# Optimization experiments

Measured on AMD Instinct MI355X. Metric: run time of the kernel, lower is better.

## Reference

```python
import jax, jax.numpy as jnp
import numpy as np

IN_SIZE = 128
OUT_SIZE = 128
NEG_SLOPE = 0.01  # flax.nnx.leaky_relu default


def setup_inputs() -> dict:
    key = jax.random.key(0)
    x = jax.random.normal(key, (8, IN_SIZE, IN_SIZE, 128), dtype=jnp.float32)
    return {"x": x}


def reference(x) -> jnp.ndarray:
    b, _, _, c = x.shape
    x = jax.image.resize(x, (b, 2 * IN_SIZE, 2 * IN_SIZE, c), method='bicubic', antialias=True)
    # filtered nonlinearity
    x = jax.nn.leaky_relu(x, negative_slope=NEG_SLOPE)
    # bicubic antialiased downsample back to out_size
    x = jax.image.resize(x, (b, OUT_SIZE, OUT_SIZE, c), method='bicubic', antialias=True)
    return x
```

## Files before the change

kernel.cpp:

```cpp
#include <hip/hip_runtime.h>

typedef float f2 __attribute__((ext_vector_type(2)));
typedef float f4 __attribute__((ext_vector_type(4)));

#define IN_H 128
#define IN_W 128
#define NCH  128
#define UPN  256

constexpr int SEG  = 8;
constexpr int COLS = 32;
constexpr int CH   = 32;
constexpr int IRW  = 14;
constexpr int ICW  = 38;
constexpr int NT4  = IRW * ICW * CH / 4;

__device__ __forceinline__ float cubic_k(float x) {
  float r = 0.f;
  if (x < 1.f)      r = (1.5f * x - 2.5f) * x * x + 1.f;
  else if (x < 2.f) r = ((-0.5f * x + 2.5f) * x - 4.f) * x + 2.f;
  return r;
}

#define GLDS(g, l)                                                         \
  __builtin_amdgcn_global_load_lds(                                        \
      (const __attribute__((address_space(1))) void*)(g),                  \
      (__attribute__((address_space(3))) void*)(l), 16, 0, 0)

__global__ __launch_bounds__(256, 2)
void actfilter_kernel(const float* __restrict__ x, float* __restrict__ out) {
  __shared__ __align__(16) float xin[IRW][ICW][CH];
  __shared__ __align__(16) float upw[UPN][4];
  __shared__ __align__(16) float dww[IN_H][8];

  const int tid = threadIdx.x;

  int bid  = blockIdx.x;
  int work = ((bid & 7) << 8) | (bid >> 3);
  const int b   = work >> 8;
  const int rs  = (work >> 4) & 15;
  const int cs  = (work >> 2) & 3;
  const int chs = work & 3;
  const int i0  = rs * SEG;
  const int jc0 = cs * COLS;
  const int c0  = chs * CH;
  const int mlo = i0 - 3;
  const int mhi = i0 + 10;

  const float* xbase = x   + (size_t)b * IN_H * IN_W * NCH;
  float*       obase = out + (size_t)b * IN_H * IN_W * NCH;

  {
    char* lbase = (char*)&xin[0][0][0] + ((tid >> 6) << 10);
#pragma unroll
    for (int pass = 0; pass < 17; ++pass) {
      int t = tid + pass * 256;
      if (t < NT4) {
        int row   = t / 304;
        int rem   = t - row * 304;
        int col   = rem >> 3;
        int piece = rem & 7;
        int gr = min(max(mlo + row, 0), IN_H - 1);
        int gc = min(max(jc0 - 3 + col, 0), IN_W - 1);
        const float* gp = xbase + ((size_t)gr * IN_W + gc) * NCH + c0 + piece * 4;
        GLDS(gp, lbase + pass * 4096);
      }
    }
  }

  {
    int o = tid;
    int k = o >> 1;
    int base = (o & 1) ? (k - 1) : (k - 2);
    float s = 0.5f * o - 0.25f;
    float w[4]; float sum = 0.f;
#pragma unroll
    for (int t = 0; t < 4; ++t) {
      int tap = base + t;
      float wt = (tap >= 0 && tap < IN_H) ? cubic_k(fabsf(s - (float)tap)) : 0.f;
      w[t] = wt; sum += wt;
    }
    float inv = 1.f / sum;
#pragma unroll
    for (int t = 0; t < 4; ++t) upw[o][t] = w[t] * inv;
  }
  if (tid < IN_H) {
    int j = tid;
    float s = 2.f * j + 0.5f;
    float w[8]; float sum = 0.f;
#pragma unroll
    for (int t = 0; t < 8; ++t) {
      int tap = 2 * j - 3 + t;
      float wt = (tap >= 0 && tap < UPN) ? cubic_k(0.5f * fabsf(s - (float)tap)) : 0.f;
      w[t] = wt; sum += wt;
    }
    float inv = 1.f / sum;
#pragma unroll
    for (int t = 0; t < 8; ++t) dww[j][t] = w[t] * inv;
  }

  __syncthreads();

  const int cp = tid >> 4;
  const int e  = tid & 15;
  const int j0 = jc0 + 2 * cp;

  f4 wvv[10];
#pragma unroll
  for (int c = 0; c < 10; ++c) {
    int cu = min(max(2 * j0 - 3 + c, 0), UPN - 1);
    wvv[c] = *(const f4*)&upw[cu][0];
  }
  float dw0[8], dw1[8];
  {
    f4 a = *(const f4*)&dww[j0][0],     bq = *(const f4*)&dww[j0][4];
    f4 c2 = *(const f4*)&dww[j0 + 1][0], d = *(const f4*)&dww[j0 + 1][4];
#pragma unroll
    for (int t = 0; t < 4; ++t) {
      dw0[t] = a[t]; dw0[t + 4] = bq[t];
      dw1[t] = c2[t]; dw1[t + 4] = d[t];
    }
  }

  const int r_lo = max(2 * i0 - 3, 0);
  const int r_hi = min(2 * i0 + 2 * SEG + 2, UPN - 1);

  const f4 whE = {-0.0234375f, 0.2265625f, 0.8671875f, -0.0703125f};
  const f4 whO = {-0.0703125f, 0.8671875f, 0.2265625f, -0.0234375f};

  f2 tw[4][10];
  f2 accA[4], accB[4];
#pragma unroll
  for (int s2 = 0; s2 < 4; ++s2) {
    accA[s2] = (f2){0.f, 0.f};
    accB[s2] = (f2){0.f, 0.f};
  }

#define DO_R(RV, WHC, S0, S1, S2, S3)                                        \
  do {                                                                       \
    int r = (RV);                                                            \
    if (r >= r_lo && r <= r_hi) {                                            \
      f4 wh = (WHC);                                                         \
      if (r < 3 || r > 252) wh = *(const f4*)&upw[r][0];                     \
      f2 z0 = (f2){0.f, 0.f}, z1 = (f2){0.f, 0.f};                           \
      _Pragma("unroll")                                                      \
      for (int c = 0; c < 10; ++c) {                                         \
        f2 hu = wh.x * tw[S0][c] + wh.y * tw[S1][c]                          \
              + wh.z * tw[S2][c] + wh.w * tw[S3][c];                         \
        f2 lv;                                                               \
        lv.x = fmaxf(hu.x, 0.01f * hu.x);                                    \
        lv.y = fmaxf(hu.y, 0.01f * hu.y);                                    \
        if (c < 8)  z0 += dw0[c] * lv;                                       \
        if (c >= 2) z1 += dw1[c - 2] * lv;                                   \
      }                                                                      \
      int ilo = max(i0, (r - 3) >> 1);                                       \
      int ihi = min(i0 + SEG - 1, (r + 3) >> 1);                             \
      _Pragma("unroll")                                                      \
      for (int s = 0; s < 4; ++s) {                                          \
        int i = ilo + ((s - ilo) & 3);                                       \
        if (i <= ihi) {                                                      \
          float w = dww[i][r - 2 * i + 3];                                   \
          accA[s] += w * z0;                                                 \
          accB[s] += w * z1;                                                 \
          bool done = (r == 2 * i + 4) ||                                    \
                      (r == UPN - 1 && 2 * i + 4 > UPN - 1);                 \
          if (done) {                                                        \
            float* dst = obase + ((size_t)i * IN_W + j0) * NCH + c0 + 2 * e; \
            *(f2*)dst         = accA[s];                                     \
            *(f2*)(dst + NCH) = accB[s];                                     \
            accA[s] = (f2){0.f, 0.f};                                        \
            accB[s] = (f2){0.f, 0.f};                                        \
          }                                                                  \
        }                                                                    \
      }                                                                      \
    }                                                                        \
  } while (0)

#define STEP(PH)                                                             \
  do {                                                                       \
    int m = mlo + mb + (PH);                                                 \
    if (m <= mhi) {                                                          \
      int ml = m - mlo;                                                      \
      f2 raw[8];                                                             \
      _Pragma("unroll")                                                      \
      for (int k = 0; k < 8; ++k)                                            \
        raw[k] = *(const f2*)&xin[ml][2 * cp + k][2 * e];                    \
      _Pragma("unroll")                                                      \
      for (int c = 0; c < 10; ++c) {                                         \
        tw[(PH) & 3][c] = wvv[c].x * raw[(c >> 1) + 0]                       \
                        + wvv[c].y * raw[(c >> 1) + 1]                       \
                        + wvv[c].z * raw[(c >> 1) + 2]                       \
                        + wvv[c].w * raw[(c >> 1) + 3];                      \
      }                                                                      \
      DO_R(2 * m - 3, whO, ((PH) + 1) & 3, ((PH) + 2) & 3, ((PH) + 3) & 3, (PH) & 3); \
      DO_R(2 * m - 2, whE, ((PH) + 1) & 3, ((PH) + 2) & 3, ((PH) + 3) & 3, (PH) & 3); \
    }                                                                        \
  } while (0)

  for (int mb = 0; mb < 16; mb += 4) {
    STEP(0);
    STEP(1);
    STEP(2);
    STEP(3);
  }

#undef STEP
#undef DO_R
}

extern "C" void kernel_launch(void* const* d_in, const int* in_sizes, int n_in,
                              void* d_out, int out_size, void* d_ws, size_t ws_size,
                              hipStream_t stream) {
  const float* x = (const float*)d_in[0];
  float* out = (float*)d_out;
  actfilter_kernel<<<dim3(2048), dim3(256), 0, stream>>>(x, out);
}
```

Before: 76.34 us.

## Stage input tile in LDS as fp16 via register loads with padded rows

Replaces the direct global-to-LDS async loads with register loads that convert the input to packed fp16 (round-toward-zero) before storing to a padded LDS tile. The loads are staged in batches interleaved with the weight-table setup to overlap latency. The intent is to halve LDS footprint and read bandwidth, possibly improving occupancy and reducing bank conflicts. It adds conversion instructions and register pressure, and loses precision by converting inputs to fp16, which may violate accuracy tolerance.

```diff
diff --git a/kernel.cpp b/kernel.cpp
--- a/kernel.cpp
+++ b/kernel.cpp
@@ -2,6 +2,7 @@
 
 typedef float f2 __attribute__((ext_vector_type(2)));
 typedef float f4 __attribute__((ext_vector_type(4)));
+typedef _Float16 h2 __attribute__((ext_vector_type(2)));
 
 #define IN_H 128
 #define IN_W 128
@@ -11,9 +12,11 @@
 constexpr int SEG  = 8;
 constexpr int COLS = 32;
 constexpr int CH   = 32;
+constexpr int CHP  = 38;
 constexpr int IRW  = 14;
 constexpr int ICW  = 38;
 constexpr int NT4  = IRW * ICW * CH / 4;
+constexpr int TPR  = ICW * CH / 4;
 
 __device__ __forceinline__ float cubic_k(float x) {
   float r = 0.f;
@@ -22,14 +25,14 @@
   return r;
 }
 
-#define GLDS(g, l)                                                         \
-  __builtin_amdgcn_global_load_lds(                                        \
-      (const __attribute__((address_space(1))) void*)(g),                  \
-      (__attribute__((address_space(3))) void*)(l), 16, 0, 0)
+__device__ __forceinline__ h2 pkrtz(float a, float b) {
+  auto t = __builtin_amdgcn_cvt_pkrtz(a, b);
+  return __builtin_bit_cast(h2, t);
+}
 
 __global__ __launch_bounds__(256, 2)
 void actfilter_kernel(const float* __restrict__ x, float* __restrict__ out) {
-  __shared__ __align__(16) float xin[IRW][ICW][CH];
+  __shared__ __align__(16) _Float16 xin[IRW][ICW][CHP];
   __shared__ __align__(16) float upw[UPN][4];
   __shared__ __align__(16) float dww[IN_H][8];
 
@@ -50,23 +53,44 @@
   const float* xbase = x   + (size_t)b * IN_H * IN_W * NCH;
   float*       obase = out + (size_t)b * IN_H * IN_W * NCH;
 
-  {
-    char* lbase = (char*)&xin[0][0][0] + ((tid >> 6) << 10);
-#pragma unroll
-    for (int pass = 0; pass < 17; ++pass) {
-      int t = tid + pass * 256;
-      if (t < NT4) {
-        int row   = t / 304;
-        int rem   = t - row * 304;
-        int col   = rem >> 3;
-        int piece = rem & 7;
-        int gr = min(max(mlo + row, 0), IN_H - 1);
-        int gc = min(max(jc0 - 3 + col, 0), IN_W - 1);
-        const float* gp = xbase + ((size_t)gr * IN_W + gc) * NCH + c0 + piece * 4;
-        GLDS(gp, lbase + pass * 4096);
+  auto ldb = [&](int base, int cnt, f4* v) {
+#pragma unroll
+    for (int k = 0; k < 6; ++k) {
+      if (k < cnt) {
+        int t = tid + (base + k) * 256;
+        if (t < NT4) {
+          int row   = t / TPR;
+          int rem   = t - row * TPR;
+          int col   = rem >> 3;
+          int piece = rem & 7;
+          int gr = min(max(mlo + row, 0), IN_H - 1);
+          int gc = min(max(jc0 - 3 + col, 0), IN_W - 1);
+          v[k] = *(const f4*)(xbase + ((size_t)gr * IN_W + gc) * NCH
+                              + c0 + piece * 4);
+        }
       }
     }
-  }
+  };
+  auto stb = [&](int base, int cnt, const f4* v) {
+#pragma unroll
+    for (int k = 0; k < 6; ++k) {
+      if (k < cnt) {
+        int t = tid + (base + k) * 256;
+        if (t < NT4) {
+          int row   = t / TPR;
+          int rem   = t - row * TPR;
+          int col   = rem >> 3;
+          int piece = rem & 7;
+          _Float16* lp = &xin[row][col][piece * 4];
+          *(h2*)lp       = pkrtz(v[k].x, v[k].y);
+          *(h2*)(lp + 2) = pkrtz(v[k].z, v[k].w);
+        }
+      }
+    }
+  };
+
+  f4 sA[6], sB[6];
+  ldb(0, 6, sA);
 
   {
     int o = tid;
@@ -84,6 +108,10 @@
 #pragma unroll
     for (int t = 0; t < 4; ++t) upw[o][t] = w[t] * inv;
   }
+
+  ldb(6, 6, sB);
+  stb(0, 6, sA);
+
   if (tid < IN_H) {
     int j = tid;
     float s = 2.f * j + 0.5f;
@@ -98,6 +126,10 @@
 #pragma unroll
     for (int t = 0; t < 8; ++t) dww[j][t] = w[t] * inv;
   }
+
+  ldb(12, 5, sA);
+  stb(6, 6, sB);
+  stb(12, 5, sA);
 
   __syncthreads();
 
@@ -183,8 +215,11 @@
       int ml = m - mlo;                                                      \
       f2 raw[8];                                                             \
       _Pragma("unroll")                                                      \
-      for (int k = 0; k < 8; ++k)                                            \
-        raw[k] = *(const f2*)&xin[ml][2 * cp + k][2 * e];                    \
+      for (int k = 0; k < 8; ++k) {                                          \
+        h2 rv = *(const h2*)&xin[ml][2 * cp + k][2 * e];                     \
+        raw[k].x = (float)rv.x;                                              \
+        raw[k].y = (float)rv.y;                                              \
+      }                                                                      \
       _Pragma("unroll")                                                      \
       for (int c = 0; c < 10; ++c) {                                         \
         tw[(PH) & 3][c] = wvv[c].x * raw[(c >> 1) + 0]                       \
```

Result: slower. 80.26 us (+5.1%).

## Remap threads to one channel by four output columns for wider horizontal reuse

Applied to the files above, without the earlier changes.

Each thread now handles one channel and four consecutive output columns instead of two channels by two columns. The horizontal upsample row of 14 taps is shared across four downsample outputs, so less of it is recomputed between neighbouring columns (10 taps per 2 columns before, 14 per 4 now). The cost is more registers per thread (tw grows to 4x14 and the accumulators to 4x4), which may lower occupancy. Loads and stores also become scalar and strided across columns instead of float2.

```diff
diff --git a/kernel.cpp b/kernel.cpp
--- a/kernel.cpp
+++ b/kernel.cpp
@@ -1,6 +1,5 @@
 #include <hip/hip_runtime.h>
 
-typedef float f2 __attribute__((ext_vector_type(2)));
 typedef float f4 __attribute__((ext_vector_type(4)));
 
 #define IN_H 128
@@ -101,25 +100,23 @@
 
   __syncthreads();
 
-  const int cp = tid >> 4;
-  const int e  = tid & 15;
-  const int j0 = jc0 + 2 * cp;
-
-  f4 wvv[10];
-#pragma unroll
-  for (int c = 0; c < 10; ++c) {
+  const int cp = tid >> 5;
+  const int e  = tid & 31;
+  const int j0 = jc0 + 4 * cp;
+
+  f4 wvv[14];
+#pragma unroll
+  for (int c = 0; c < 14; ++c) {
     int cu = min(max(2 * j0 - 3 + c, 0), UPN - 1);
     wvv[c] = *(const f4*)&upw[cu][0];
   }
-  float dw0[8], dw1[8];
-  {
-    f4 a = *(const f4*)&dww[j0][0],     bq = *(const f4*)&dww[j0][4];
-    f4 c2 = *(const f4*)&dww[j0 + 1][0], d = *(const f4*)&dww[j0 + 1][4];
-#pragma unroll
-    for (int t = 0; t < 4; ++t) {
-      dw0[t] = a[t]; dw0[t + 4] = bq[t];
-      dw1[t] = c2[t]; dw1[t + 4] = d[t];
-    }
+  float dw[4][8];
+#pragma unroll
+  for (int q = 0; q < 4; ++q) {
+    f4 lo = *(const f4*)&dww[j0 + q][0];
+    f4 hi = *(const f4*)&dww[j0 + q][4];
+#pragma unroll
+    for (int t = 0; t < 4; ++t) { dw[q][t] = lo[t]; dw[q][t + 4] = hi[t]; }
   }
 
   const int r_lo = max(2 * i0 - 3, 0);
@@ -128,13 +125,12 @@
   const f4 whE = {-0.0234375f, 0.2265625f, 0.8671875f, -0.0703125f};
   const f4 whO = {-0.0703125f, 0.8671875f, 0.2265625f, -0.0234375f};
 
-  f2 tw[4][10];
-  f2 accA[4], accB[4];
-#pragma unroll
-  for (int s2 = 0; s2 < 4; ++s2) {
-    accA[s2] = (f2){0.f, 0.f};
-    accB[s2] = (f2){0.f, 0.f};
-  }
+  float tw[4][14];
+  float acc[4][4];
+#pragma unroll
+  for (int s2 = 0; s2 < 4; ++s2)
+#pragma unroll
+    for (int q = 0; q < 4; ++q) acc[s2][q] = 0.f;
 
 #define DO_R(RV, WHC, S0, S1, S2, S3)                                        \
   do {                                                                       \
@@ -142,16 +138,20 @@
     if (r >= r_lo && r <= r_hi) {                                            \
       f4 wh = (WHC);                                                         \
       if (r < 3 || r > 252) wh = *(const f4*)&upw[r][0];                     \
-      f2 z0 = (f2){0.f, 0.f}, z1 = (f2){0.f, 0.f};                           \
-      _Pragma("unroll")                                                      \
-      for (int c = 0; c < 10; ++c) {                                         \
-        f2 hu = wh.x * tw[S0][c] + wh.y * tw[S1][c]                          \
-              + wh.z * tw[S2][c] + wh.w * tw[S3][c];                         \
-        f2 lv;                                                               \
-        lv.x = fmaxf(hu.x, 0.01f * hu.x);                                    \
-        lv.y = fmaxf(hu.y, 0.01f * hu.y);                                    \
-        if (c < 8)  z0 += dw0[c] * lv;                                       \
-        if (c >= 2) z1 += dw1[c - 2] * lv;                                   \
+      float lv[14];                                                          \
+      _Pragma("unroll")                                                      \
+      for (int c = 0; c < 14; ++c) {                                         \
+        float hu = wh.x * tw[S0][c] + wh.y * tw[S1][c]                       \
+                 + wh.z * tw[S2][c] + wh.w * tw[S3][c];                      \
+        lv[c] = fmaxf(hu, 0.01f * hu);                                       \
+      }                                                                      \
+      float z[4];                                                            \
+      _Pragma("unroll")                                                      \
+      for (int q = 0; q < 4; ++q) {                                          \
+        float zq = dw[q][0] * lv[2 * q];                                     \
+        _Pragma("unroll")                                                    \
+        for (int t = 1; t < 8; ++t) zq += dw[q][t] * lv[2 * q + t];          \
+        z[q] = zq;                                                           \
       }                                                                      \
       int ilo = max(i0, (r - 3) >> 1);                                       \
       int ihi = min(i0 + SEG - 1, (r + 3) >> 1);                             \
@@ -160,16 +160,17 @@
         int i = ilo + ((s - ilo) & 3);                                       \
         if (i <= ihi) {                                                      \
           float w = dww[i][r - 2 * i + 3];                                   \
-          accA[s] += w * z0;                                                 \
-          accB[s] += w * z1;                                                 \
+          _Pragma("unroll")                                                  \
+          for (int q = 0; q < 4; ++q) acc[s][q] += w * z[q];                 \
           bool done = (r == 2 * i + 4) ||                                    \
                       (r == UPN - 1 && 2 * i + 4 > UPN - 1);                 \
           if (done) {                                                        \
-            float* dst = obase + ((size_t)i * IN_W + j0) * NCH + c0 + 2 * e; \
-            *(f2*)dst         = accA[s];                                     \
-            *(f2*)(dst + NCH) = accB[s];                                     \
-            accA[s] = (f2){0.f, 0.f};                                        \
-            accB[s] = (f2){0.f, 0.f};                                        \
+            float* dst = obase + ((size_t)i * IN_W + j0) * NCH + c0 + e;     \
+            _Pragma("unroll")                                                \
+            for (int q = 0; q < 4; ++q) {                                    \
+              dst[q * NCH] = acc[s][q];                                      \
+              acc[s][q] = 0.f;                                               \
+            }                                                                \
           }                                                                  \
         }                                                                    \
       }                                                                      \
@@ -181,12 +182,12 @@
     int m = mlo + mb + (PH);                                                 \
     if (m <= mhi) {                                                          \
       int ml = m - mlo;                                                      \
-      f2 raw[8];                                                             \
-      _Pragma("unroll")                                                      \
-      for (int k = 0; k < 8; ++k)                                            \
-        raw[k] = *(const f2*)&xin[ml][2 * cp + k][2 * e];                    \
-      _Pragma("unroll")                                                      \
-      for (int c = 0; c < 10; ++c) {                                         \
+      float raw[10];                                                         \
+      _Pragma("unroll")                                                      \
+      for (int k = 0; k < 10; ++k)                                           \
+        raw[k] = xin[ml][4 * cp + k][e];                                     \
+      _Pragma("unroll")                                                      \
+      for (int c = 0; c < 14; ++c) {                                         \
         tw[(PH) & 3][c] = wvv[c].x * raw[(c >> 1) + 0]                       \
                         + wvv[c].y * raw[(c >> 1) + 1]                       \
                         + wvv[c].z * raw[(c >> 1) + 2]                       \
```

After: 96.50 us. 1.26x slower.
